# Kernel tuning notes

Measured on AMD Instinct MI355X. Metric: run time of the kernel, lower is better.

Reference implementation:

```python
import jax, jax.numpy as jnp
import numpy as np

N, F_IN, F_OUT = 8192, 256, 128
ALPHA = 0.2  # LeakyReLU negative slope
NEG_INF = -9e15


def setup_inputs() -> dict:
    key = jax.random.key(0)
    k1, k2, k3, k4 = jax.random.split(key, 4)
    h = jax.random.normal(k1, (N, F_IN), dtype=jnp.float32)
    adj = jax.random.randint(k2, (N, N), 0, 2, dtype=jnp.int32)
    # Xavier-uniform-like init (gain=1.414)
    lim_w = 1.414 * np.sqrt(6.0 / (F_IN + F_OUT))
    W = jax.random.uniform(k3, (F_IN, F_OUT), dtype=jnp.float32, minval=-lim_w, maxval=lim_w)
    lim_a = 1.414 * np.sqrt(6.0 / (2 * F_OUT + 1))
    a = jax.random.uniform(k4, (2 * F_OUT, 1), dtype=jnp.float32, minval=-lim_a, maxval=lim_a)
    return {"h": h, "adj": adj, "W": W, "a": a}


def reference(h, adj, W, a):
    # Wh: [N, F_OUT]
    Wh = h @ W
    f_out = W.shape[1]
    # The torch code builds an [N, N, 2F] concat tensor; mathematically
    # e_ij = leakyrelu(a1 . Wh_i + a2 . Wh_j), so compute via two projections.
    a1 = a[:f_out, 0]   # [F_OUT]
    a2 = a[f_out:, 0]   # [F_OUT]
    f1 = Wh @ a1        # [N]
    f2 = Wh @ a2        # [N]
    e = jax.nn.leaky_relu(f1[:, None] + f2[None, :], negative_slope=ALPHA)  # [N, N]
    e = jnp.where(adj > 0, e, NEG_INF)
    attention = jax.nn.softmax(e, axis=1)  # [N, N]; dropout p=0 (eval mode)
    h_prime = attention @ Wh               # [N, F_OUT]
    return jax.nn.elu(h_prime)
```

## Files before the change

kernel.cpp:

```cpp
#include <hip/hip_runtime.h>
#include <hip/hip_bf16.h>
#include <math.h>

typedef short short8 __attribute__((ext_vector_type(8)));
typedef float f32x4 __attribute__((ext_vector_type(4)));
typedef int i32x4 __attribute__((ext_vector_type(4)));

#define NN 8192
#define FIN 256
#define FOUT 128
#define LRELU_A 0.2f
#define L2E 1.44269504088896f

__device__ __forceinline__ short f2bf(float x) {
    unsigned u = __builtin_bit_cast(unsigned, x);
    unsigned r = (u + 0x7FFFu + ((u >> 16) & 1u)) >> 16;
    return (short)r;
}

__global__ __launch_bounds__(256) void k_wh(const float* __restrict__ h,
                                            const float* __restrict__ W,
                                            const float* __restrict__ a,
                                            float* __restrict__ Wh,
                                            float* __restrict__ f1,
                                            float* __restrict__ f2) {
    __shared__ float hs[8][FIN];
    const int tid = threadIdx.x;
    const int r0 = blockIdx.x * 8;
    #pragma unroll
    for (int i = 0; i < 2; ++i) {
        int f4 = tid + 256 * i;
        int row = f4 >> 6;
        int k4 = (f4 & 63) << 2;
        *(float4*)&hs[row][k4] = *(const float4*)(h + (size_t)(r0 + row) * FIN + k4);
    }
    __syncthreads();
    const int c4 = (tid & 31) * 4;
    const int row = tid >> 5;
    float acc0 = 0.f, acc1 = 0.f, acc2 = 0.f, acc3 = 0.f;
    #pragma unroll 4
    for (int k = 0; k < FIN; ++k) {
        float hv = hs[row][k];
        float4 w4 = *(const float4*)(W + (size_t)k * FOUT + c4);
        acc0 = fmaf(hv, w4.x, acc0);
        acc1 = fmaf(hv, w4.y, acc1);
        acc2 = fmaf(hv, w4.z, acc2);
        acc3 = fmaf(hv, w4.w, acc3);
    }
    float4 o; o.x = acc0; o.y = acc1; o.z = acc2; o.w = acc3;
    *(float4*)(Wh + (size_t)(r0 + row) * FOUT + c4) = o;

    float4 a1v = *(const float4*)(a + c4);
    float4 a2v = *(const float4*)(a + FOUT + c4);
    float p1 = acc0 * a1v.x + acc1 * a1v.y + acc2 * a1v.z + acc3 * a1v.w;
    float p2 = acc0 * a2v.x + acc1 * a2v.y + acc2 * a2v.z + acc3 * a2v.w;
    #pragma unroll
    for (int m = 1; m <= 16; m <<= 1) {
        p1 += __shfl_xor(p1, m, 64);
        p2 += __shfl_xor(p2, m, 64);
    }
    if ((tid & 31) == 0) {
        f1[r0 + row] = p1;
        f2[r0 + row] = p2;
    }
}

__global__ __launch_bounds__(256) void k_transpose(const float* __restrict__ Wh,
                                                   short* __restrict__ WhT) {
    __shared__ float t32[32][33];
    const int tid = threadIdx.x;
    const int tx = tid & 31, ty = tid >> 5;
    const int rb = (blockIdx.x & 255) * 32;
    const int cb = (blockIdx.x >> 8) * 32;
    #pragma unroll
    for (int q = 0; q < 4; ++q) {
        int r = ty + q * 8;
        t32[r][tx] = Wh[(size_t)(rb + r) * FOUT + cb + tx];
    }
    __syncthreads();
    #pragma unroll
    for (int q = 0; q < 4; ++q) {
        int c = ty + q * 8;
        WhT[(size_t)(cb + c) * NN + rb + tx] = f2bf(t32[tx][c]);
    }
}

__global__ __launch_bounds__(256) void k_gmax(const float* __restrict__ f2,
                                              float* __restrict__ gmax) {
    const int tid = threadIdx.x;
    float m = -1e30f;
    for (int i = tid; i < NN; i += 256) m = fmaxf(m, f2[i]);
    #pragma unroll
    for (int s = 1; s <= 32; s <<= 1) m = fmaxf(m, __shfl_xor(m, s, 64));
    __shared__ float red[4];
    if ((tid & 63) == 0) red[tid >> 6] = m;
    __syncthreads();
    if (tid == 0) gmax[0] = fmaxf(fmaxf(red[0], red[1]), fmaxf(red[2], red[3]));
}

__device__ __forceinline__ void gat_body(const short* __restrict__ lrd, unsigned m8,
                                         float4 fa, float4 fb,
                                         float f1r, float mh2, float& den,
                                         f32x4 acc[8]) {
    short8 b0 = *(const short8*)(lrd + 0 * 1024);
    short8 b1 = *(const short8*)(lrd + 1 * 1024);
    short8 b2 = *(const short8*)(lrd + 2 * 1024);
    short8 b3 = *(const short8*)(lrd + 3 * 1024);
    short8 b4 = *(const short8*)(lrd + 4 * 1024);
    short8 b5 = *(const short8*)(lrd + 5 * 1024);
    short8 b6 = *(const short8*)(lrd + 6 * 1024);
    short8 b7 = *(const short8*)(lrd + 7 * 1024);

    float fv[8] = {fa.x, fa.y, fa.z, fa.w, fb.x, fb.y, fb.z, fb.w};
    short8 af;
    #pragma unroll
    for (int i = 0; i < 8; ++i) {
        float e = f1r + fv[i];
        e = fmaxf(e, LRELU_A * e);
        float p = __builtin_amdgcn_exp2f(fmaf(e, L2E, -mh2));
        p = (m8 & (1u << i)) ? p : 0.0f;
        den += p;
        af[i] = f2bf(p);
    }
    acc[0] = __builtin_amdgcn_mfma_f32_16x16x32_bf16(af, b0, acc[0], 0, 0, 0);
    acc[1] = __builtin_amdgcn_mfma_f32_16x16x32_bf16(af, b1, acc[1], 0, 0, 0);
    acc[2] = __builtin_amdgcn_mfma_f32_16x16x32_bf16(af, b2, acc[2], 0, 0, 0);
    acc[3] = __builtin_amdgcn_mfma_f32_16x16x32_bf16(af, b3, acc[3], 0, 0, 0);
    acc[4] = __builtin_amdgcn_mfma_f32_16x16x32_bf16(af, b4, acc[4], 0, 0, 0);
    acc[5] = __builtin_amdgcn_mfma_f32_16x16x32_bf16(af, b5, acc[5], 0, 0, 0);
    acc[6] = __builtin_amdgcn_mfma_f32_16x16x32_bf16(af, b6, acc[6], 0, 0, 0);
    acc[7] = __builtin_amdgcn_mfma_f32_16x16x32_bf16(af, b7, acc[7], 0, 0, 0);
}

#define GAT_STEP(KOFF, X0, X1, X2, X3, LRD0, LRD1, WDST)                           \
    {                                                                              \
        const int koff_ = (KOFF);                                                  \
        float4 fa0 = *(const float4*)(f2p + koff_);                                \
        float4 fb0 = *(const float4*)(f2p + koff_ + 4);                            \
        float4 fa1 = *(const float4*)(f2p + koff_ + 32);                           \
        float4 fb1 = *(const float4*)(f2p + koff_ + 36);                           \
        unsigned m0 = (unsigned)(X0.x & 1)        | ((unsigned)(X0.y & 1) << 1) |  \
                      ((unsigned)(X0.z & 1) << 2) | ((unsigned)(X0.w & 1) << 3) |  \
                      ((unsigned)(X1.x & 1) << 4) | ((unsigned)(X1.y & 1) << 5) |  \
                      ((unsigned)(X1.z & 1) << 6) | ((unsigned)(X1.w & 1) << 7);   \
        unsigned m1 = (unsigned)(X2.x & 1)        | ((unsigned)(X2.y & 1) << 1) |  \
                      ((unsigned)(X2.z & 1) << 2) | ((unsigned)(X2.w & 1) << 3) |  \
                      ((unsigned)(X3.x & 1) << 4) | ((unsigned)(X3.y & 1) << 5) |  \
                      ((unsigned)(X3.z & 1) << 6) | ((unsigned)(X3.w & 1) << 7);   \
        const int kst_ = (koff_ + 64 < kchunk) ? koff_ + 64 : 0;                   \
        short8 r0 = *(const short8*)(wsrc + kst_);                                 \
        short8 r1 = *(const short8*)(wsrc + kst_ + 32 * NN);                       \
        short8 r2 = *(const short8*)(wsrc + kst_ + 64 * NN);                       \
        short8 r3 = *(const short8*)(wsrc + kst_ + 96 * NN);                       \
        const int kpre_ = (koff_ + 128 < kchunk) ? koff_ + 128 : 0;                \
        X0 = *(const i32x4*)(adjp + kpre_);                                        \
        X1 = *(const i32x4*)(adjp + kpre_ + 4);                                    \
        X2 = *(const i32x4*)(adjp + kpre_ + 32);                                   \
        X3 = *(const i32x4*)(adjp + kpre_ + 36);                                   \
        gat_body(LRD0, m0, fa0, fb0, f1r, mh2, den, acc);                          \
        gat_body(LRD1, m1, fa1, fb1, f1r, mh2, den, acc);                          \
        *(short8*)(WDST) = r0;                                                     \
        *(short8*)(WDST + 2048) = r1;                                              \
        *(short8*)(WDST + 4096) = r2;                                              \
        *(short8*)(WDST + 6144) = r3;                                              \
        asm volatile("s_waitcnt lgkmcnt(0)" ::: "memory");                         \
        __builtin_amdgcn_s_barrier();                                              \
    }

__global__ __launch_bounds__(256, 3) void k_attn(const int* __restrict__ adj,
                                                 const short* __restrict__ WhT,
                                                 const float* __restrict__ f1,
                                                 const float* __restrict__ f2,
                                                 const float* __restrict__ gmax,
                                                 float* __restrict__ numb,
                                                 float* __restrict__ denb,
                                                 int kchunk, int nsplit) {
    __shared__ __align__(16) short ldsW[2][8192];
    const int tid = threadIdx.x;
    const int lane = tid & 63;
    const int wave = tid >> 6;
    const int split = blockIdx.x & (nsplit - 1);
    const int rt = blockIdx.x / nsplit;
    const int rowbase = rt * 64 + wave * 16;
    const int col = lane & 15;
    const int kg = lane >> 4;
    const int arow = rowbase + col;

    const float f1r = f1[arow];
    const float gm = gmax[0];
    const float t0v = f1r + gm;
    const float mhat = fmaxf(t0v, LRELU_A * t0v);
    const float mh2 = mhat * L2E;

    const int kbase0 = split * kchunk;
    const float* f2p = f2 + kbase0 + kg * 8;
    const int* adjp = adj + (size_t)arow * NN + kbase0 + kg * 8;

    const int tq = tid >> 3;
    const int ts = tid & 7;
    const short* wsrc = WhT + (size_t)tq * NN + kbase0 + ts * 8;
    short* wdst0 = &ldsW[0][tq * 64 + ((ts ^ (tq & 7)) * 8)];
    short* wdst1 = &ldsW[1][tq * 64 + ((ts ^ (tq & 7)) * 8)];

    const short* lrdE0 = &ldsW[0][col * 64 + ((kg ^ (col & 7)) * 8)];
    const short* lrdE1 = &ldsW[0][col * 64 + (((kg ^ (col & 7)) * 8) ^ 32)];
    const short* lrdO0 = lrdE0 + 8192;
    const short* lrdO1 = lrdE1 + 8192;

    f32x4 acc[8] = {};
    float den = 0.0f;

    {
        short8 r0 = *(const short8*)(wsrc);
        short8 r1 = *(const short8*)(wsrc + 32 * NN);
        short8 r2 = *(const short8*)(wsrc + 64 * NN);
        short8 r3 = *(const short8*)(wsrc + 96 * NN);
        *(short8*)(wdst0) = r0;
        *(short8*)(wdst0 + 2048) = r1;
        *(short8*)(wdst0 + 4096) = r2;
        *(short8*)(wdst0 + 6144) = r3;
    }
    i32x4 xa0 = *(const i32x4*)(adjp + 0);
    i32x4 xa1 = *(const i32x4*)(adjp + 4);
    i32x4 xa2 = *(const i32x4*)(adjp + 32);
    i32x4 xa3 = *(const i32x4*)(adjp + 36);
    i32x4 xb0 = *(const i32x4*)(adjp + 64);
    i32x4 xb1 = *(const i32x4*)(adjp + 68);
    i32x4 xb2 = *(const i32x4*)(adjp + 96);
    i32x4 xb3 = *(const i32x4*)(adjp + 100);
    asm volatile("s_waitcnt lgkmcnt(0)" ::: "memory");
    __builtin_amdgcn_s_barrier();

    for (int koff = 0; koff < kchunk; koff += 128) {
        GAT_STEP(koff,      xa0, xa1, xa2, xa3, lrdE0, lrdE1, wdst1);
        GAT_STEP(koff + 64, xb0, xb1, xb2, xb3, lrdO0, lrdO1, wdst0);
    }

    den += __shfl_xor(den, 16, 64);
    den += __shfl_xor(den, 32, 64);
    if (lane < 16) denb[(size_t)split * NN + rowbase + lane] = den;

    float* np = numb + ((size_t)split * NN + rowbase) * FOUT;
    const int rsub = (lane >> 4) * 4;
    #pragma unroll
    for (int t = 0; t < 8; ++t) {
        #pragma unroll
        for (int r = 0; r < 4; ++r) {
            np[(size_t)(rsub + r) * FOUT + t * 16 + col] = acc[t][r];
        }
    }
}

__global__ __launch_bounds__(256) void k_final(const float* __restrict__ numb,
                                               const float* __restrict__ denb,
                                               float* __restrict__ out,
                                               int splitk) {
    const int idx = blockIdx.x * 256 + threadIdx.x;
    const int row = idx >> 7;
    float s = 0.0f, d = 0.0f;
    for (int sp = 0; sp < splitk; ++sp) {
        s += numb[((size_t)sp * NN) * FOUT + idx];
        d += denb[(size_t)sp * NN + row];
    }
    float v = s / d;
    out[idx] = v > 0.0f ? v : expm1f(v);
}

extern "C" void kernel_launch(void* const* d_in, const int* in_sizes, int n_in,
                              void* d_out, int out_size, void* d_ws, size_t ws_size,
                              hipStream_t stream) {
    const float* h = (const float*)d_in[0];
    const int* adj = (const int*)d_in[1];
    const float* W = (const float*)d_in[2];
    const float* a = (const float*)d_in[3];
    float* out = (float*)d_out;

    char* ws = (char*)d_ws;
    size_t off = 0;
    auto alloc = [&](size_t nbytes) {
        char* p = ws + off;
        off = (off + nbytes + 255) & ~(size_t)255;
        return p;
    };
    float* Wh  = (float*)alloc((size_t)NN * FOUT * 4);
    short* WhT = (short*)alloc((size_t)FOUT * NN * 2);
    float* f1  = (float*)alloc(NN * 4);
    float* f2  = (float*)alloc(NN * 4);
    float* gmx = (float*)alloc(256);

    int splitk = 8;
    while (splitk > 1 &&
           off + (size_t)splitk * ((size_t)NN * FOUT * 4 + NN * 4 + 512) > ws_size)
        splitk >>= 1;
    float* numb = (float*)alloc((size_t)splitk * NN * FOUT * 4);
    float* denb = (float*)alloc((size_t)splitk * NN * 4);
    const int kchunk = NN / splitk;

    k_wh<<<NN / 8, 256, 0, stream>>>(h, W, a, Wh, f1, f2);
    k_transpose<<<(NN / 32) * (FOUT / 32), 256, 0, stream>>>(Wh, WhT);
    k_gmax<<<1, 256, 0, stream>>>(f2, gmx);
    k_attn<<<(NN / 64) * splitk, 256, 0, stream>>>(adj, WhT, f1, f2, gmx, numb, denb,
                                                   kchunk, splitk);
    k_final<<<NN * FOUT / 256, 256, 0, stream>>>(numb, denb, out, splitk);
}
```

Measured before the change: 142.0 us.

## Stage WhT tiles via global_load_lds direct-to-LDS and raise occupancy

Replaces the register round-trip staging of WhT tiles (global load into VGPRs, then ds_write) with global_load_lds DMA straight into the swizzled LDS double buffer. The swizzle moves to the global source address. Waits switch from lgkmcnt to vmcnt counts, and sched_barriers pin the instruction order. This frees the staging registers, so launch bounds go up to 4 blocks per SIMD. The risk is that the vmcnt counts must exactly match the outstanding adj and LDS loads, or reads could be stale.

```diff
diff --git a/kernel.cpp b/kernel.cpp
--- a/kernel.cpp
+++ b/kernel.cpp
@@ -16,6 +16,12 @@
     unsigned u = __builtin_bit_cast(unsigned, x);
     unsigned r = (u + 0x7FFFu + ((u >> 16) & 1u)) >> 16;
     return (short)r;
+}
+
+__device__ __forceinline__ void gload_lds16(const void* g, void* l) {
+    __builtin_amdgcn_global_load_lds(
+        (const __attribute__((address_space(1))) void*)g,
+        (__attribute__((address_space(3))) void*)l, 16, 0, 0);
 }
 
 __global__ __launch_bounds__(256) void k_wh(const float* __restrict__ h,
@@ -132,7 +138,15 @@
     acc[7] = __builtin_amdgcn_mfma_f32_16x16x32_bf16(af, b7, acc[7], 0, 0, 0);
 }
 
-#define GAT_STEP(KOFF, X0, X1, X2, X3, LRD0, LRD1, WDST)                           \
+#define STAGE(LB, KC)                                          \
+    do {                                                       \
+        gload_lds16(gsrc0 + (KC),           (LB) + 0 * 512);   \
+        gload_lds16(gsrc0 + (KC) + 8 * NN,  (LB) + 1 * 512);   \
+        gload_lds16(gsrc0 + (KC) + 16 * NN, (LB) + 2 * 512);   \
+        gload_lds16(gsrc0 + (KC) + 24 * NN, (LB) + 3 * 512);   \
+    } while (0)
+
+#define GAT_STEP(KOFF, X0, X1, X2, X3, LRD0, LRD1, LWB)                            \
     {                                                                              \
         const int koff_ = (KOFF);                                                  \
         float4 fa0 = *(const float4*)(f2p + koff_);                                \
@@ -147,27 +161,23 @@
                       ((unsigned)(X2.z & 1) << 2) | ((unsigned)(X2.w & 1) << 3) |  \
                       ((unsigned)(X3.x & 1) << 4) | ((unsigned)(X3.y & 1) << 5) |  \
                       ((unsigned)(X3.z & 1) << 6) | ((unsigned)(X3.w & 1) << 7);   \
+        __builtin_amdgcn_sched_barrier(0);                                         \
         const int kst_ = (koff_ + 64 < kchunk) ? koff_ + 64 : 0;                   \
-        short8 r0 = *(const short8*)(wsrc + kst_);                                 \
-        short8 r1 = *(const short8*)(wsrc + kst_ + 32 * NN);                       \
-        short8 r2 = *(const short8*)(wsrc + kst_ + 64 * NN);                       \
-        short8 r3 = *(const short8*)(wsrc + kst_ + 96 * NN);                       \
+        STAGE(LWB, kst_);                                                          \
+        __builtin_amdgcn_sched_barrier(0);                                         \
         const int kpre_ = (koff_ + 128 < kchunk) ? koff_ + 128 : 0;                \
         X0 = *(const i32x4*)(adjp + kpre_);                                        \
         X1 = *(const i32x4*)(adjp + kpre_ + 4);                                    \
         X2 = *(const i32x4*)(adjp + kpre_ + 32);                                   \
         X3 = *(const i32x4*)(adjp + kpre_ + 36);                                   \
+        __builtin_amdgcn_sched_barrier(0);                                         \
         gat_body(LRD0, m0, fa0, fb0, f1r, mh2, den, acc);                          \
         gat_body(LRD1, m1, fa1, fb1, f1r, mh2, den, acc);                          \
-        *(short8*)(WDST) = r0;                                                     \
-        *(short8*)(WDST + 2048) = r1;                                              \
-        *(short8*)(WDST + 4096) = r2;                                              \
-        *(short8*)(WDST + 6144) = r3;                                              \
-        asm volatile("s_waitcnt lgkmcnt(0)" ::: "memory");                         \
+        asm volatile("s_waitcnt vmcnt(4)" ::: "memory");                           \
         __builtin_amdgcn_s_barrier();                                              \
     }
 
-__global__ __launch_bounds__(256, 3) void k_attn(const int* __restrict__ adj,
+__global__ __launch_bounds__(256, 4) void k_attn(const int* __restrict__ adj,
                                                  const short* __restrict__ WhT,
                                                  const float* __restrict__ f1,
                                                  const float* __restrict__ f2,
@@ -196,11 +206,11 @@
     const float* f2p = f2 + kbase0 + kg * 8;
     const int* adjp = adj + (size_t)arow * NN + kbase0 + kg * 8;
 
-    const int tq = tid >> 3;
-    const int ts = tid & 7;
-    const short* wsrc = WhT + (size_t)tq * NN + kbase0 + ts * 8;
-    short* wdst0 = &ldsW[0][tq * 64 + ((ts ^ (tq & 7)) * 8)];
-    short* wdst1 = &ldsW[1][tq * 64 + ((ts ^ (tq & 7)) * 8)];
+    const int srow = lane >> 3;
+    const int scol = (lane & 7) ^ srow;
+    const short* gsrc0 = WhT + (size_t)(wave * 32 + srow) * NN + kbase0 + scol * 8;
+    short* ldst0 = &ldsW[0][(wave * 32) * 64];
+    short* ldst1 = &ldsW[1][(wave * 32) * 64];
 
     const short* lrdE0 = &ldsW[0][col * 64 + ((kg ^ (col & 7)) * 8)];
     const short* lrdE1 = &ldsW[0][col * 64 + (((kg ^ (col & 7)) * 8) ^ 32)];
@@ -210,16 +220,8 @@
     f32x4 acc[8] = {};
     float den = 0.0f;
 
-    {
-        short8 r0 = *(const short8*)(wsrc);
-        short8 r1 = *(const short8*)(wsrc + 32 * NN);
-        short8 r2 = *(const short8*)(wsrc + 64 * NN);
-        short8 r3 = *(const short8*)(wsrc + 96 * NN);
-        *(short8*)(wdst0) = r0;
-        *(short8*)(wdst0 + 2048) = r1;
-        *(short8*)(wdst0 + 4096) = r2;
-        *(short8*)(wdst0 + 6144) = r3;
-    }
+    STAGE(ldst0, 0);
+    __builtin_amdgcn_sched_barrier(0);
     i32x4 xa0 = *(const i32x4*)(adjp + 0);
     i32x4 xa1 = *(const i32x4*)(adjp + 4);
     i32x4 xa2 = *(const i32x4*)(adjp + 32);
@@ -228,12 +230,13 @@
     i32x4 xb1 = *(const i32x4*)(adjp + 68);
     i32x4 xb2 = *(const i32x4*)(adjp + 96);
     i32x4 xb3 = *(const i32x4*)(adjp + 100);
-    asm volatile("s_waitcnt lgkmcnt(0)" ::: "memory");
+    __builtin_amdgcn_sched_barrier(0);
+    asm volatile("s_waitcnt vmcnt(8)" ::: "memory");
     __builtin_amdgcn_s_barrier();
 
     for (int koff = 0; koff < kchunk; koff += 128) {
-        GAT_STEP(koff,      xa0, xa1, xa2, xa3, lrdE0, lrdE1, wdst1);
-        GAT_STEP(koff + 64, xb0, xb1, xb2, xb3, lrdO0, lrdO1, wdst0);
+        GAT_STEP(koff,      xa0, xa1, xa2, xa3, lrdE0, lrdE1, ldst1);
+        GAT_STEP(koff + 64, xb0, xb1, xb2, xb3, lrdO0, lrdO1, ldst0);
     }
 
     den += __shfl_xor(den, 16, 64);
```

New measurement: 191.5 us. 34.8% more time.

## Pre-pack adjacency into bitmask kernel and stream packed bits in attention

Applied to the files above, without the earlier changes.

Adds a k_pack kernel that reads the int32 adjacency matrix once and writes a 1-bit-per-entry mask. The attention kernel then loads 64-bit mask words instead of int32 adjacency vectors, and prefetches f2 one step ahead instead of loading it in place. Launch bounds rise to 4 blocks per SM. The intent is to shrink the attention kernel's memory stream and register pressure. The catch is that the full adjacency read now happens in a separate kernel, so it can no longer overlap with the attention compute.

```diff
diff --git a/kernel.cpp b/kernel.cpp
--- a/kernel.cpp
+++ b/kernel.cpp
@@ -16,6 +16,23 @@
     unsigned u = __builtin_bit_cast(unsigned, x);
     unsigned r = (u + 0x7FFFu + ((u >> 16) & 1u)) >> 16;
     return (short)r;
+}
+
+__global__ __launch_bounds__(256) void k_pack(const int* __restrict__ adj,
+                                              unsigned* __restrict__ packed) {
+    const int row = blockIdx.x;
+    const int t = threadIdx.x;
+    const int* p = adj + (size_t)row * NN + t * 32;
+    unsigned m = 0;
+    #pragma unroll
+    for (int q = 0; q < 8; ++q) {
+        i32x4 v = __builtin_nontemporal_load((const i32x4*)(p + q * 4));
+        m |= (v.x != 0 ? 1u : 0u) << (q * 4 + 0);
+        m |= (v.y != 0 ? 1u : 0u) << (q * 4 + 1);
+        m |= (v.z != 0 ? 1u : 0u) << (q * 4 + 2);
+        m |= (v.w != 0 ? 1u : 0u) << (q * 4 + 3);
+    }
+    packed[(size_t)row * (NN / 32) + t] = m;
 }
 
 __global__ __launch_bounds__(256) void k_wh(const float* __restrict__ h,
@@ -132,33 +149,21 @@
     acc[7] = __builtin_amdgcn_mfma_f32_16x16x32_bf16(af, b7, acc[7], 0, 0, 0);
 }
 
-#define GAT_STEP(KOFF, X0, X1, X2, X3, LRD0, LRD1, WDST)                           \
+#define GAT_STEP(KOFF, CM, CF0, CF1, CF2, CF3, NM, NF0, NF1, NF2, NF3, LRD0, LRD1, WDST) \
     {                                                                              \
         const int koff_ = (KOFF);                                                  \
-        float4 fa0 = *(const float4*)(f2p + koff_);                                \
-        float4 fb0 = *(const float4*)(f2p + koff_ + 4);                            \
-        float4 fa1 = *(const float4*)(f2p + koff_ + 32);                           \
-        float4 fb1 = *(const float4*)(f2p + koff_ + 36);                           \
-        unsigned m0 = (unsigned)(X0.x & 1)        | ((unsigned)(X0.y & 1) << 1) |  \
-                      ((unsigned)(X0.z & 1) << 2) | ((unsigned)(X0.w & 1) << 3) |  \
-                      ((unsigned)(X1.x & 1) << 4) | ((unsigned)(X1.y & 1) << 5) |  \
-                      ((unsigned)(X1.z & 1) << 6) | ((unsigned)(X1.w & 1) << 7);   \
-        unsigned m1 = (unsigned)(X2.x & 1)        | ((unsigned)(X2.y & 1) << 1) |  \
-                      ((unsigned)(X2.z & 1) << 2) | ((unsigned)(X2.w & 1) << 3) |  \
-                      ((unsigned)(X3.x & 1) << 4) | ((unsigned)(X3.y & 1) << 5) |  \
-                      ((unsigned)(X3.z & 1) << 6) | ((unsigned)(X3.w & 1) << 7);   \
         const int kst_ = (koff_ + 64 < kchunk) ? koff_ + 64 : 0;                   \
         short8 r0 = *(const short8*)(wsrc + kst_);                                 \
         short8 r1 = *(const short8*)(wsrc + kst_ + 32 * NN);                       \
         short8 r2 = *(const short8*)(wsrc + kst_ + 64 * NN);                       \
         short8 r3 = *(const short8*)(wsrc + kst_ + 96 * NN);                       \
-        const int kpre_ = (koff_ + 128 < kchunk) ? koff_ + 128 : 0;                \
-        X0 = *(const i32x4*)(adjp + kpre_);                                        \
-        X1 = *(const i32x4*)(adjp + kpre_ + 4);                                    \
-        X2 = *(const i32x4*)(adjp + kpre_ + 32);                                   \
-        X3 = *(const i32x4*)(adjp + kpre_ + 36);                                   \
-        gat_body(LRD0, m0, fa0, fb0, f1r, mh2, den, acc);                          \
-        gat_body(LRD1, m1, fa1, fb1, f1r, mh2, den, acc);                          \
+        NM  = *(const uint2*)(pkrow + (kst_ >> 5));                                \
+        NF0 = *(const float4*)(f2p + kst_);                                        \
+        NF1 = *(const float4*)(f2p + kst_ + 4);                                    \
+        NF2 = *(const float4*)(f2p + kst_ + 32);                                   \
+        NF3 = *(const float4*)(f2p + kst_ + 36);                                   \
+        gat_body(LRD0, (CM.x >> mshift) & 0xffu, CF0, CF1, f1r, mh2, den, acc);    \
+        gat_body(LRD1, (CM.y >> mshift) & 0xffu, CF2, CF3, f1r, mh2, den, acc);    \
         *(short8*)(WDST) = r0;                                                     \
         *(short8*)(WDST + 2048) = r1;                                              \
         *(short8*)(WDST + 4096) = r2;                                              \
@@ -167,7 +172,7 @@
         __builtin_amdgcn_s_barrier();                                              \
     }
 
-__global__ __launch_bounds__(256, 3) void k_attn(const int* __restrict__ adj,
+__global__ __launch_bounds__(256, 4) void k_attn(const unsigned* __restrict__ packed,
                                                  const short* __restrict__ WhT,
                                                  const float* __restrict__ f1,
                                                  const float* __restrict__ f2,
@@ -194,7 +199,8 @@
 
     const int kbase0 = split * kchunk;
     const float* f2p = f2 + kbase0 + kg * 8;
-    const int* adjp = adj + (size_t)arow * NN + kbase0 + kg * 8;
+    const unsigned* pkrow = packed + (size_t)arow * (NN / 32) + (kbase0 >> 5);
+    const int mshift = kg * 8;
 
     const int tq = tid >> 3;
     const int ts = tid & 7;
@@ -220,20 +226,21 @@
         *(short8*)(wdst0 + 4096) = r2;
         *(short8*)(wdst0 + 6144) = r3;
     }
-    i32x4 xa0 = *(const i32x4*)(adjp + 0);
-    i32x4 xa1 = *(const i32x4*)(adjp + 4);
-    i32x4 xa2 = *(const i32x4*)(adjp + 32);
-    i32x4 xa3 = *(const i32x4*)(adjp + 36);
-    i32x4 xb0 = *(const i32x4*)(adjp + 64);
-    i32x4 xb1 = *(const i32x4*)(adjp + 68);
-    i32x4 xb2 = *(const i32x4*)(adjp + 96);
-    i32x4 xb3 = *(const i32x4*)(adjp + 100);
+    uint2  mE  = *(const uint2*)(pkrow);
+    float4 fE0 = *(const float4*)(f2p);
+    float4 fE1 = *(const float4*)(f2p + 4);
+    float4 fE2 = *(const float4*)(f2p + 32);
+    float4 fE3 = *(const float4*)(f2p + 36);
+    uint2  mO;
+    float4 fO0, fO1, fO2, fO3;
     asm volatile("s_waitcnt lgkmcnt(0)" ::: "memory");
     __builtin_amdgcn_s_barrier();
 
     for (int koff = 0; koff < kchunk; koff += 128) {
-        GAT_STEP(koff,      xa0, xa1, xa2, xa3, lrdE0, lrdE1, wdst1);
-        GAT_STEP(koff + 64, xb0, xb1, xb2, xb3, lrdO0, lrdO1, wdst0);
+        GAT_STEP(koff,      mE, fE0, fE1, fE2, fE3, mO, fO0, fO1, fO2, fO3,
+                 lrdE0, lrdE1, wdst1);
+        GAT_STEP(koff + 64, mO, fO0, fO1, fO2, fO3, mE, fE0, fE1, fE2, fE3,
+                 lrdO0, lrdO1, wdst0);
     }
 
     den += __shfl_xor(den, 16, 64);
@@ -282,11 +289,12 @@
         off = (off + nbytes + 255) & ~(size_t)255;
         return p;
     };
-    float* Wh  = (float*)alloc((size_t)NN * FOUT * 4);
-    short* WhT = (short*)alloc((size_t)FOUT * NN * 2);
-    float* f1  = (float*)alloc(NN * 4);
-    float* f2  = (float*)alloc(NN * 4);
-    float* gmx = (float*)alloc(256);
+    float* Wh      = (float*)alloc((size_t)NN * FOUT * 4);
+    short* WhT     = (short*)alloc((size_t)FOUT * NN * 2);
+    float* f1      = (float*)alloc(NN * 4);
+    float* f2      = (float*)alloc(NN * 4);
+    float* gmx     = (float*)alloc(256);
+    unsigned* pkd  = (unsigned*)alloc((size_t)NN * (NN / 32) * 4);
 
     int splitk = 8;
     while (splitk > 1 &&
@@ -296,10 +304,11 @@
     float* denb = (float*)alloc((size_t)splitk * NN * 4);
     const int kchunk = NN / splitk;
 
+    k_pack<<<NN, 256, 0, stream>>>(adj, pkd);
     k_wh<<<NN / 8, 256, 0, stream>>>(h, W, a, Wh, f1, f2);
     k_transpose<<<(NN / 32) * (FOUT / 32), 256, 0, stream>>>(Wh, WhT);
     k_gmax<<<1, 256, 0, stream>>>(f2, gmx);
-    k_attn<<<(NN / 64) * splitk, 256, 0, stream>>>(adj, WhT, f1, f2, gmx, numb, denb,
+    k_attn<<<(NN / 64) * splitk, 256, 0, stream>>>(pkd, WhT, f1, f2, gmx, numb, denb,
                                                    kchunk, splitk);
     k_final<<<NN * FOUT / 256, 256, 0, stream>>>(numb, denb, out, splitk);
 }
```

After: 204.3 us. +43.9%, slower.

## Stage f2 chunk in LDS, remap WhT staging loads, raise occupancy hint

Applied to the files above, without the earlier changes.

Preloads the block's slice of f2 into shared memory once instead of re-reading it from global memory every step. It also remaps the WhT tile staging so each group of four lanes reads 64 contiguous bytes from a row, covering two row pairs with swizzled LDS destinations. The adjacency prefetch is issued before the WhT loads, and the launch bound asks for 4 blocks per CU instead of 3. The extra 8KB of LDS and the tighter register budget could limit the occupancy gain or cause register spills.

```diff
diff --git a/kernel.cpp b/kernel.cpp
--- a/kernel.cpp
+++ b/kernel.cpp
@@ -132,13 +132,13 @@
     acc[7] = __builtin_amdgcn_mfma_f32_16x16x32_bf16(af, b7, acc[7], 0, 0, 0);
 }
 
-#define GAT_STEP(KOFF, X0, X1, X2, X3, LRD0, LRD1, WDST)                           \
+#define GAT_STEP(KOFF, X0, X1, X2, X3, LRD0, LRD1, BUFW)                           \
     {                                                                              \
         const int koff_ = (KOFF);                                                  \
-        float4 fa0 = *(const float4*)(f2p + koff_);                                \
-        float4 fb0 = *(const float4*)(f2p + koff_ + 4);                            \
-        float4 fa1 = *(const float4*)(f2p + koff_ + 32);                           \
-        float4 fb1 = *(const float4*)(f2p + koff_ + 36);                           \
+        float4 fa0 = *(const float4*)(lf2 + koff_);                                \
+        float4 fb0 = *(const float4*)(lf2 + koff_ + 4);                            \
+        float4 fa1 = *(const float4*)(lf2 + koff_ + 32);                           \
+        float4 fb1 = *(const float4*)(lf2 + koff_ + 36);                           \
         unsigned m0 = (unsigned)(X0.x & 1)        | ((unsigned)(X0.y & 1) << 1) |  \
                       ((unsigned)(X0.z & 1) << 2) | ((unsigned)(X0.w & 1) << 3) |  \
                       ((unsigned)(X1.x & 1) << 4) | ((unsigned)(X1.y & 1) << 5) |  \
@@ -147,27 +147,27 @@
                       ((unsigned)(X2.z & 1) << 2) | ((unsigned)(X2.w & 1) << 3) |  \
                       ((unsigned)(X3.x & 1) << 4) | ((unsigned)(X3.y & 1) << 5) |  \
                       ((unsigned)(X3.z & 1) << 6) | ((unsigned)(X3.w & 1) << 7);   \
-        const int kst_ = (koff_ + 64 < kchunk) ? koff_ + 64 : 0;                   \
-        short8 r0 = *(const short8*)(wsrc + kst_);                                 \
-        short8 r1 = *(const short8*)(wsrc + kst_ + 32 * NN);                       \
-        short8 r2 = *(const short8*)(wsrc + kst_ + 64 * NN);                       \
-        short8 r3 = *(const short8*)(wsrc + kst_ + 96 * NN);                       \
         const int kpre_ = (koff_ + 128 < kchunk) ? koff_ + 128 : 0;                \
         X0 = *(const i32x4*)(adjp + kpre_);                                        \
         X1 = *(const i32x4*)(adjp + kpre_ + 4);                                    \
         X2 = *(const i32x4*)(adjp + kpre_ + 32);                                   \
         X3 = *(const i32x4*)(adjp + kpre_ + 36);                                   \
+        const int kst_ = (koff_ + 64 < kchunk) ? koff_ + 64 : 0;                   \
+        short8 r0 = *(const short8*)(g00 + kst_);                                  \
+        short8 r1 = *(const short8*)(g01 + kst_);                                  \
+        short8 r2 = *(const short8*)(g10 + kst_);                                  \
+        short8 r3 = *(const short8*)(g11 + kst_);                                  \
         gat_body(LRD0, m0, fa0, fb0, f1r, mh2, den, acc);                          \
         gat_body(LRD1, m1, fa1, fb1, f1r, mh2, den, acc);                          \
-        *(short8*)(WDST) = r0;                                                     \
-        *(short8*)(WDST + 2048) = r1;                                              \
-        *(short8*)(WDST + 4096) = r2;                                              \
-        *(short8*)(WDST + 6144) = r3;                                              \
+        *(short8*)((BUFW) + d00) = r0;                                             \
+        *(short8*)((BUFW) + d01) = r1;                                             \
+        *(short8*)((BUFW) + d10) = r2;                                             \
+        *(short8*)((BUFW) + d11) = r3;                                             \
         asm volatile("s_waitcnt lgkmcnt(0)" ::: "memory");                         \
         __builtin_amdgcn_s_barrier();                                              \
     }
 
-__global__ __launch_bounds__(256, 3) void k_attn(const int* __restrict__ adj,
+__global__ __launch_bounds__(256, 4) void k_attn(const int* __restrict__ adj,
                                                  const short* __restrict__ WhT,
                                                  const float* __restrict__ f1,
                                                  const float* __restrict__ f2,
@@ -176,6 +176,7 @@
                                                  float* __restrict__ denb,
                                                  int kchunk, int nsplit) {
     __shared__ __align__(16) short ldsW[2][8192];
+    __shared__ __align__(16) float ldsF2[2048];
     const int tid = threadIdx.x;
     const int lane = tid & 63;
     const int wave = tid >> 6;
@@ -193,14 +194,22 @@
     const float mh2 = mhat * L2E;
 
     const int kbase0 = split * kchunk;
-    const float* f2p = f2 + kbase0 + kg * 8;
     const int* adjp = adj + (size_t)arow * NN + kbase0 + kg * 8;
-
-    const int tq = tid >> 3;
-    const int ts = tid & 7;
-    const short* wsrc = WhT + (size_t)tq * NN + kbase0 + ts * 8;
-    short* wdst0 = &ldsW[0][tq * 64 + ((ts ^ (tq & 7)) * 8)];
-    short* wdst1 = &ldsW[1][tq * 64 + ((ts ^ (tq & 7)) * 8)];
+    const float* lf2 = ldsF2 + kg * 8;
+
+    const int srow = wave * 32 + (lane >> 2);
+    const int sx = srow & 7;
+    const short* gsb = WhT + (size_t)srow * NN + kbase0 + (lane & 3) * 8;
+    const short* g00 = gsb;
+    const short* g01 = gsb + 32;
+    const short* g10 = gsb + (size_t)16 * NN;
+    const short* g11 = gsb + (size_t)16 * NN + 32;
+    const int d00 = srow * 64        + ((((lane & 3) + 0) ^ sx) * 8);
+    const int d01 = srow * 64        + ((((lane & 3) + 4) ^ sx) * 8);
+    const int d10 = (srow + 16) * 64 + ((((lane & 3) + 0) ^ sx) * 8);
+    const int d11 = (srow + 16) * 64 + ((((lane & 3) + 4) ^ sx) * 8);
+    short* buf0 = &ldsW[0][0];
+    short* buf1 = &ldsW[1][0];
 
     const short* lrdE0 = &ldsW[0][col * 64 + ((kg ^ (col & 7)) * 8)];
     const short* lrdE1 = &ldsW[0][col * 64 + (((kg ^ (col & 7)) * 8) ^ 32)];
@@ -210,15 +219,17 @@
     f32x4 acc[8] = {};
     float den = 0.0f;
 
+    for (int i = tid * 4; i < kchunk; i += 1024)
+        *(float4*)&ldsF2[i] = *(const float4*)(f2 + kbase0 + i);
     {
-        short8 r0 = *(const short8*)(wsrc);
-        short8 r1 = *(const short8*)(wsrc + 32 * NN);
-        short8 r2 = *(const short8*)(wsrc + 64 * NN);
-        short8 r3 = *(const short8*)(wsrc + 96 * NN);
-        *(short8*)(wdst0) = r0;
-        *(short8*)(wdst0 + 2048) = r1;
-        *(short8*)(wdst0 + 4096) = r2;
-        *(short8*)(wdst0 + 6144) = r3;
+        short8 r0 = *(const short8*)(g00);
+        short8 r1 = *(const short8*)(g01);
+        short8 r2 = *(const short8*)(g10);
+        short8 r3 = *(const short8*)(g11);
+        *(short8*)(buf0 + d00) = r0;
+        *(short8*)(buf0 + d01) = r1;
+        *(short8*)(buf0 + d10) = r2;
+        *(short8*)(buf0 + d11) = r3;
     }
     i32x4 xa0 = *(const i32x4*)(adjp + 0);
     i32x4 xa1 = *(const i32x4*)(adjp + 4);
@@ -232,8 +243,8 @@
     __builtin_amdgcn_s_barrier();
 
     for (int koff = 0; koff < kchunk; koff += 128) {
-        GAT_STEP(koff,      xa0, xa1, xa2, xa3, lrdE0, lrdE1, wdst1);
-        GAT_STEP(koff + 64, xb0, xb1, xb2, xb3, lrdO0, lrdO1, wdst0);
+        GAT_STEP(koff,      xa0, xa1, xa2, xa3, lrdE0, lrdE1, buf1);
+        GAT_STEP(koff + 64, xb0, xb1, xb2, xb3, lrdO0, lrdO1, buf0);
     }
 
     den += __shfl_xor(den, 16, 64);
```

Result: slower. 150.9 us (+6.2%).
